# Performance work log

Measured on AMD Instinct MI355X. Metric: run time of the kernel, lower is better.

## Reference

```python
import jax, jax.numpy as jnp
import numpy as np

B, S, D = 4, 2048, 256


def setup_inputs() -> dict:
    key = jax.random.key(0)
    ks = jax.random.split(key, 8)
    context = jax.random.normal(ks[0], (B, S, D), dtype=jnp.float32)
    eos_mask = jax.random.randint(ks[1], (B, S, S), 0, 2, dtype=jnp.int32)
    prior = jax.random.uniform(ks[2], (B, S, S), dtype=jnp.float32)
    Wq = jax.random.normal(ks[3], (D, D), dtype=jnp.float32) * 0.02
    bq = jnp.zeros((D,), dtype=jnp.float32)
    Wk = jax.random.normal(ks[4], (D, D), dtype=jnp.float32) * 0.02
    bk = jnp.zeros((D,), dtype=jnp.float32)
    ln_a = jnp.ones((D,), dtype=jnp.float32)
    ln_b = jnp.zeros((D,), dtype=jnp.float32)
    return {"context": context, "prior": prior, "Wq": Wq, "bq": bq,
            "Wk": Wk, "bk": bk, "ln_a": ln_a, "ln_b": ln_b,
            "eos_mask": eos_mask}


def reference(context, prior, Wq, bq, Wk, bk, ln_a, ln_b, eos_mask):
    seq = context.shape[1]
    # LayerNorm (torch: unbiased std, eps added to std)
    mean = context.mean(axis=-1, keepdims=True)
    std = jnp.std(context, axis=-1, ddof=1, keepdims=True)
    x = ln_a * (context - mean) / (std + 1e-6) + ln_b

    idx = jnp.arange(seq)
    diff = idx[None, :] - idx[:, None]
    a = diff == 1                      # superdiagonal
    offdiag = jnp.abs(diff) == 1       # a + c (super + sub diagonal)
    eye = diff == 0                    # b
    tri = jnp.triu(jnp.ones((seq, seq), dtype=jnp.float32))

    # mask = eos_mask & (a + c)  (precedence: & binds looser than +)
    mask = jnp.bitwise_and(eos_mask, offdiag.astype(jnp.int32))

    # torch Linear: y = x @ W.T + b
    query = x @ Wq.T + bq
    key = x @ Wk.T + bk
    scores = jnp.einsum('bqd,bkd->bqk', query, key) / 256.0
    scores = jnp.where(mask == 0, -1e9, scores)
    neibor = jax.nn.softmax(scores, axis=-1)
    neibor = jnp.sqrt(neibor * neibor.transpose(0, 2, 1) + 1e-9)
    neibor = prior + (1.0 - prior) * neibor

    # log -> zero except superdiagonal -> triangular matmul -> exp
    t = jnp.where(a, jnp.log(neibor + 1e-9), 0.0) @ tri   # [B,S,S]
    g = jnp.exp(jnp.matmul(tri, t))                        # [B,S,S]
    strict_upper = jnp.logical_and(tri.astype(bool), jnp.logical_not(eye))
    g = jnp.where(strict_upper, g, 0.0)  # masked_fill(tri - b == 0, 0)
    g = g + g.transpose(0, 2, 1) + jnp.where(eye, neibor, 1e-9)
    return g
```

## Files before the change

kernel.cpp:

```cpp
#include <hip/hip_runtime.h>
#include <math.h>

#define SS 2048
#define DD 256
#define NB 4
#define NR (NB * SS)

__device__ __forceinline__ float block_sum(float v, float* sh) {
    int lane = threadIdx.x & 63;
    int wave = threadIdx.x >> 6;
#pragma unroll
    for (int off = 32; off > 0; off >>= 1) v += __shfl_down(v, off, 64);
    if (lane == 0) sh[wave] = v;
    __syncthreads();
    float r = sh[0] + sh[1] + sh[2] + sh[3];
    __syncthreads();
    return r;
}

__global__ __launch_bounds__(256) void prep_kernel(
    const float* __restrict__ Wq, const float* __restrict__ Wk,
    const float* __restrict__ bq, float* __restrict__ A, float* __restrict__ u) {
    int t = threadIdx.x;
    int d = blockIdx.x;
    if (d < DD) {
        float acc = 0.0f;
        for (int i = 0; i < DD; i++) acc += Wq[i * DD + d] * Wk[i * DD + t];
        A[d * DD + t] = acc;
    } else {
        float acc = 0.0f;
        for (int i = 0; i < DD; i++) acc += Wk[i * DD + t] * bq[i];
        u[t] = acc;
    }
}

__global__ __launch_bounds__(256) void ln_kernel(
    const float* __restrict__ ctx, const float* __restrict__ ln_a,
    const float* __restrict__ ln_b, float* __restrict__ xn) {
    __shared__ float sh[4];
    int r = blockIdx.x, t = threadIdx.x;
    float v = ctx[r * DD + t];
    float mean = block_sum(v, sh) * (1.0f / 256.0f);
    float d = v - mean;
    float s2 = block_sum(d * d, sh) * (1.0f / 255.0f);
    float inv = 1.0f / (sqrtf(s2) + 1e-6f);
    xn[r * DD + t] = ln_a[t] * d * inv + ln_b[t];
}

#define BM 64
#define BN 64
#define BK 16
__global__ __launch_bounds__(256) void gemm_kernel(
    const float* __restrict__ X, const float* __restrict__ A,
    const float* __restrict__ u, float* __restrict__ Y) {
    __shared__ float Xs[BK][BM + 1];
    __shared__ float As[BK][BN];
    int tid = threadIdx.x;
    int row0 = blockIdx.x * BM;
    int col0 = blockIdx.y * BN;
    int tx = tid & 15, ty = tid >> 4;
    float acc[4][4] = {};
    for (int k0 = 0; k0 < DD; k0 += BK) {
        {
            int m = tid >> 2;
            int kq = (tid & 3) * 4;
            float4 x4 = *(const float4*)(X + (size_t)(row0 + m) * DD + k0 + kq);
            Xs[kq + 0][m] = x4.x; Xs[kq + 1][m] = x4.y;
            Xs[kq + 2][m] = x4.z; Xs[kq + 3][m] = x4.w;
        }
        {
            int k = tid >> 4;
            int nq = (tid & 15) * 4;
            float4 a4 = *(const float4*)(A + (size_t)(k0 + k) * DD + col0 + nq);
            *(float4*)&As[k][nq] = a4;
        }
        __syncthreads();
#pragma unroll
        for (int k = 0; k < BK; k++) {
            float a[4], b[4];
#pragma unroll
            for (int i = 0; i < 4; i++) a[i] = Xs[k][ty * 4 + i];
#pragma unroll
            for (int j = 0; j < 4; j++) b[j] = As[k][tx * 4 + j];
#pragma unroll
            for (int i = 0; i < 4; i++)
#pragma unroll
                for (int j = 0; j < 4; j++) acc[i][j] += a[i] * b[j];
        }
        __syncthreads();
    }
    float4 uv = *(const float4*)(u + col0 + tx * 4);
#pragma unroll
    for (int i = 0; i < 4; i++) {
        float4 o = make_float4(acc[i][0] + uv.x, acc[i][1] + uv.y,
                               acc[i][2] + uv.z, acc[i][3] + uv.w);
        *(float4*)(Y + (size_t)(row0 + ty * 4 + i) * DD + col0 + tx * 4) = o;
    }
}

__global__ __launch_bounds__(256) void score_kernel(
    const float* __restrict__ Y, const float* __restrict__ xn,
    const int* __restrict__ eos, float4* __restrict__ pvals) {
    __shared__ float sh[4];
    int r = blockIdx.x, t = threadIdx.x;
    int s = r & (SS - 1), b = r >> 11;
    float yv = Y[(size_t)r * DD + t];
    bool has_n = (s < SS - 1), has_p = (s > 0);
    float xnext = has_n ? xn[(size_t)(r + 1) * DD + t] : 0.0f;
    float xprev = has_p ? xn[(size_t)(r - 1) * DD + t] : 0.0f;
    float dn = block_sum(yv * xnext, sh);
    float dp = block_sum(yv * xprev, sh);
    if (t == 0) {
        size_t base = (size_t)b * SS * SS + (size_t)s * SS;
        bool mn = has_n && ((eos[base + s + 1] & 1) != 0);
        bool mp = has_p && ((eos[base + s - 1] & 1) != 0);
        float pn, pp, pd;
        if (mn && mp) {
            float d = (dn - dp) * (1.0f / 256.0f);
            pn = 1.0f / (1.0f + expf(-d));
            pp = 1.0f / (1.0f + expf(d));
            pd = 0.0f;
        } else if (mn) { pn = 1.0f; pp = 0.0f; pd = 0.0f; }
        else if (mp)   { pn = 0.0f; pp = 1.0f; pd = 0.0f; }
        else           { pn = pp = pd = (1.0f / 2048.0f); }
        pvals[r] = make_float4(pn, pp, pd, 0.0f);
    }
}

__global__ __launch_bounds__(256) void scan_kernel(
    const float4* __restrict__ pvals, const float* __restrict__ prior,
    float* __restrict__ P) {
    int b = blockIdx.x, t = threadIdx.x;
    int base_s = t * 8;
    double loc[8];
    double run = 0.0;
#pragma unroll
    for (int i = 0; i < 8; i++) {
        loc[i] = run;
        int s = base_s + i;
        float lv = 0.0f;
        if (s < SS - 1) {
            int r = b * SS + s;
            float4 pv = pvals[r];
            float4 pv1 = pvals[r + 1];
            float ns = sqrtf(pv.x * pv1.y + 1e-9f);
            float pr = prior[(size_t)b * SS * SS + (size_t)s * SS + s + 1];
            float neib = pr + (1.0f - pr) * ns;
            lv = logf(neib + 1e-9f);
        }
        run += (double)lv;
    }
    int lane = t & 63, wave = t >> 6;
    double v = run;
#pragma unroll
    for (int off = 1; off < 64; off <<= 1) {
        double uu = __shfl_up(v, off, 64);
        if (lane >= off) v += uu;
    }
    __shared__ double wsum[4];
    if (lane == 63) wsum[wave] = v;
    __syncthreads();
    double woff = 0.0;
    for (int w = 0; w < wave; w++) woff += wsum[w];
    double texcl = woff + (v - run);
#pragma unroll
    for (int i = 0; i < 8; i++)
        P[b * SS + base_s + i] = (float)(texcl + loc[i]);
}

__global__ __launch_bounds__(256) void fill_kernel(
    const float* __restrict__ P, const float4* __restrict__ pvals,
    const float* __restrict__ prior, float* __restrict__ out) {
    int blk = blockIdx.x;
    int i = blk & (SS - 1), b = blk >> 11;
    int t = threadIdx.x;
    __shared__ float shPi, shDv;
    if (t == 0) {
        shPi = P[blk];
        float pd = pvals[blk].z;
        float prd = prior[(size_t)b * SS * SS + (size_t)i * SS + i];
        shDv = prd + (1.0f - prd) * sqrtf(pd * pd + 1e-9f);
    }
    __syncthreads();
    float Pi = shPi, dv = shDv;
    const float* Pb = P + b * SS;
    size_t outbase = (size_t)blk * SS;
    float4 pj0 = *(const float4*)(Pb + t * 8);
    float4 pj1 = *(const float4*)(Pb + t * 8 + 4);
    float pj[8] = {pj0.x, pj0.y, pj0.z, pj0.w, pj1.x, pj1.y, pj1.z, pj1.w};
    float res[8];
#pragma unroll
    for (int k = 0; k < 8; k++) {
        int j = t * 8 + k;
        float d = (j > i) ? (pj[k] - Pi) : (Pi - pj[k]);
        float val = expf(d) + 1e-9f;
        res[k] = (j == i) ? dv : val;
    }
    *(float4*)(out + outbase + t * 8) = make_float4(res[0], res[1], res[2], res[3]);
    *(float4*)(out + outbase + t * 8 + 4) = make_float4(res[4], res[5], res[6], res[7]);
}

extern "C" void kernel_launch(void* const* d_in, const int* in_sizes, int n_in,
                              void* d_out, int out_size, void* d_ws, size_t ws_size,
                              hipStream_t stream) {
    const float* context = (const float*)d_in[0];
    const float* prior   = (const float*)d_in[1];
    const float* Wq      = (const float*)d_in[2];
    const float* bq      = (const float*)d_in[3];
    const float* Wk      = (const float*)d_in[4];
    const float* ln_a    = (const float*)d_in[6];
    const float* ln_b    = (const float*)d_in[7];
    const int*   eos     = (const int*)d_in[8];
    float* out = (float*)d_out;

    float* ws = (float*)d_ws;
    float* xn    = ws;
    float* Y     = ws + 2097152;
    float* A     = ws + 4194304;
    float* u     = ws + 4259840;
    float4* pv   = (float4*)(ws + 4260096);
    float* P     = ws + 4292864;

    prep_kernel<<<DD + 1, 256, 0, stream>>>(Wq, Wk, bq, A, u);
    ln_kernel<<<NR, 256, 0, stream>>>(context, ln_a, ln_b, xn);
    gemm_kernel<<<dim3(NR / BM, DD / BN), 256, 0, stream>>>(xn, A, u, Y);
    score_kernel<<<NR, 256, 0, stream>>>(Y, xn, eos, pv);
    scan_kernel<<<NB, 256, 0, stream>>>(pv, prior, P);
    fill_kernel<<<NR, 256, 0, stream>>>(P, pv, prior, out);
}
```

Measured before the change: 226.8 us.

## Fuse projection GEMM with neighbor score dot products, wave-per-row layernorm

The projection GEMM and the neighbor score kernel are merged, so each block computes full 256-wide rows of Y and immediately dots them with (x_next - x_prev). This removes the Y intermediate buffer round trip and one launch. LayerNorm now uses one wave per row with float4 loads and shuffle reductions instead of block-wide shared-memory syncs, and expf is replaced by __expf in the fill and sigmoid paths. The eos mask test drops the &1 check and the fused GEMM gets less parallelism, with only 256 blocks.

```diff
diff --git a/kernel.cpp b/kernel.cpp
--- a/kernel.cpp
+++ b/kernel.cpp
@@ -5,18 +5,6 @@
 #define DD 256
 #define NB 4
 #define NR (NB * SS)
-
-__device__ __forceinline__ float block_sum(float v, float* sh) {
-    int lane = threadIdx.x & 63;
-    int wave = threadIdx.x >> 6;
-#pragma unroll
-    for (int off = 32; off > 0; off >>= 1) v += __shfl_down(v, off, 64);
-    if (lane == 0) sh[wave] = v;
-    __syncthreads();
-    float r = sh[0] + sh[1] + sh[2] + sh[3];
-    __syncthreads();
-    return r;
-}
 
 __global__ __launch_bounds__(256) void prep_kernel(
     const float* __restrict__ Wq, const float* __restrict__ Wk,
@@ -35,95 +23,115 @@
 }
 
 __global__ __launch_bounds__(256) void ln_kernel(
-    const float* __restrict__ ctx, const float* __restrict__ ln_a,
-    const float* __restrict__ ln_b, float* __restrict__ xn) {
-    __shared__ float sh[4];
-    int r = blockIdx.x, t = threadIdx.x;
-    float v = ctx[r * DD + t];
-    float mean = block_sum(v, sh) * (1.0f / 256.0f);
-    float d = v - mean;
-    float s2 = block_sum(d * d, sh) * (1.0f / 255.0f);
-    float inv = 1.0f / (sqrtf(s2) + 1e-6f);
-    xn[r * DD + t] = ln_a[t] * d * inv + ln_b[t];
-}
-
-#define BM 64
-#define BN 64
-#define BK 16
-__global__ __launch_bounds__(256) void gemm_kernel(
+    const float4* __restrict__ ctx4, const float4* __restrict__ ln_a4,
+    const float4* __restrict__ ln_b4, float4* __restrict__ xn4) {
+    int lane = threadIdx.x & 63;
+    int wave = threadIdx.x >> 6;
+    int r = blockIdx.x * 4 + wave;
+    float4 v = ctx4[(size_t)r * 64 + lane];
+    float s = v.x + v.y + v.z + v.w;
+#pragma unroll
+    for (int off = 32; off > 0; off >>= 1) s += __shfl_xor(s, off, 64);
+    float mean = s * (1.0f / 256.0f);
+    float4 d = make_float4(v.x - mean, v.y - mean, v.z - mean, v.w - mean);
+    float s2 = d.x * d.x + d.y * d.y + d.z * d.z + d.w * d.w;
+#pragma unroll
+    for (int off = 32; off > 0; off >>= 1) s2 += __shfl_xor(s2, off, 64);
+    float inv = 1.0f / (sqrtf(s2 * (1.0f / 255.0f)) + 1e-6f);
+    float4 ga = ln_a4[lane], gb = ln_b4[lane];
+    xn4[(size_t)r * 64 + lane] = make_float4(
+        ga.x * d.x * inv + gb.x, ga.y * d.y * inv + gb.y,
+        ga.z * d.z * inv + gb.z, ga.w * d.w * inv + gb.w);
+}
+
+#define BK 32
+#define FMA4(accv, a, bv) \
+    accv.x += (a) * bv.x; accv.y += (a) * bv.y; \
+    accv.z += (a) * bv.z; accv.w += (a) * bv.w;
+
+__global__ __launch_bounds__(256) void gemm_score_kernel(
     const float* __restrict__ X, const float* __restrict__ A,
-    const float* __restrict__ u, float* __restrict__ Y) {
-    __shared__ float Xs[BK][BM + 1];
-    __shared__ float As[BK][BN];
+    const float* __restrict__ u, const int* __restrict__ eos,
+    float4* __restrict__ pvals) {
+    __shared__ float Xs[BK][33];
+    __shared__ float As[BK][256];
     int tid = threadIdx.x;
-    int row0 = blockIdx.x * BM;
-    int col0 = blockIdx.y * BN;
     int tx = tid & 15, ty = tid >> 4;
-    float acc[4][4] = {};
+    int row0 = blockIdx.x * 32;
+    const float4* X4 = (const float4*)X;
+    const float4* A4 = (const float4*)A;
+
+    float4 acc[2][4] = {};
     for (int k0 = 0; k0 < DD; k0 += BK) {
         {
-            int m = tid >> 2;
-            int kq = (tid & 3) * 4;
-            float4 x4 = *(const float4*)(X + (size_t)(row0 + m) * DD + k0 + kq);
+            int m = tid >> 3;
+            int kq = (tid & 7) * 4;
+            float4 x4 = X4[(size_t)(row0 + m) * 64 + (k0 >> 2) + (tid & 7)];
             Xs[kq + 0][m] = x4.x; Xs[kq + 1][m] = x4.y;
             Xs[kq + 2][m] = x4.z; Xs[kq + 3][m] = x4.w;
         }
-        {
-            int k = tid >> 4;
-            int nq = (tid & 15) * 4;
-            float4 a4 = *(const float4*)(A + (size_t)(k0 + k) * DD + col0 + nq);
-            *(float4*)&As[k][nq] = a4;
+#pragma unroll
+        for (int q = 0; q < 8; q++) {
+            int f4 = q * 256 + tid;
+            int k = f4 >> 6, c4 = f4 & 63;
+            *(float4*)&As[k][c4 * 4] = A4[(size_t)(k0 + k) * 64 + c4];
         }
         __syncthreads();
 #pragma unroll
         for (int k = 0; k < BK; k++) {
-            float a[4], b[4];
-#pragma unroll
-            for (int i = 0; i < 4; i++) a[i] = Xs[k][ty * 4 + i];
-#pragma unroll
-            for (int j = 0; j < 4; j++) b[j] = As[k][tx * 4 + j];
-#pragma unroll
-            for (int i = 0; i < 4; i++)
-#pragma unroll
-                for (int j = 0; j < 4; j++) acc[i][j] += a[i] * b[j];
+            float a0 = Xs[k][ty * 2];
+            float a1 = Xs[k][ty * 2 + 1];
+            float4 b0 = *(const float4*)&As[k][tx * 4];
+            float4 b1 = *(const float4*)&As[k][tx * 4 + 64];
+            float4 b2 = *(const float4*)&As[k][tx * 4 + 128];
+            float4 b3 = *(const float4*)&As[k][tx * 4 + 192];
+            FMA4(acc[0][0], a0, b0) FMA4(acc[0][1], a0, b1)
+            FMA4(acc[0][2], a0, b2) FMA4(acc[0][3], a0, b3)
+            FMA4(acc[1][0], a1, b0) FMA4(acc[1][1], a1, b1)
+            FMA4(acc[1][2], a1, b2) FMA4(acc[1][3], a1, b3)
         }
         __syncthreads();
     }
-    float4 uv = *(const float4*)(u + col0 + tx * 4);
-#pragma unroll
-    for (int i = 0; i < 4; i++) {
-        float4 o = make_float4(acc[i][0] + uv.x, acc[i][1] + uv.y,
-                               acc[i][2] + uv.z, acc[i][3] + uv.w);
-        *(float4*)(Y + (size_t)(row0 + ty * 4 + i) * DD + col0 + tx * 4) = o;
-    }
-}
-
-__global__ __launch_bounds__(256) void score_kernel(
-    const float* __restrict__ Y, const float* __restrict__ xn,
-    const int* __restrict__ eos, float4* __restrict__ pvals) {
-    __shared__ float sh[4];
-    int r = blockIdx.x, t = threadIdx.x;
-    int s = r & (SS - 1), b = r >> 11;
-    float yv = Y[(size_t)r * DD + t];
-    bool has_n = (s < SS - 1), has_p = (s > 0);
-    float xnext = has_n ? xn[(size_t)(r + 1) * DD + t] : 0.0f;
-    float xprev = has_p ? xn[(size_t)(r - 1) * DD + t] : 0.0f;
-    float dn = block_sum(yv * xnext, sh);
-    float dp = block_sum(yv * xprev, sh);
-    if (t == 0) {
-        size_t base = (size_t)b * SS * SS + (size_t)s * SS;
-        bool mn = has_n && ((eos[base + s + 1] & 1) != 0);
-        bool mp = has_p && ((eos[base + s - 1] & 1) != 0);
-        float pn, pp, pd;
-        if (mn && mp) {
-            float d = (dn - dp) * (1.0f / 256.0f);
-            pn = 1.0f / (1.0f + expf(-d));
-            pp = 1.0f / (1.0f + expf(d));
-            pd = 0.0f;
-        } else if (mn) { pn = 1.0f; pp = 0.0f; pd = 0.0f; }
-        else if (mp)   { pn = 0.0f; pp = 1.0f; pd = 0.0f; }
-        else           { pn = pp = pd = (1.0f / 2048.0f); }
-        pvals[r] = make_float4(pn, pp, pd, 0.0f);
+    const float4* u4 = (const float4*)u;
+#pragma unroll
+    for (int q = 0; q < 4; q++) {
+        float4 uv = u4[q * 16 + tx];
+        acc[0][q].x += uv.x; acc[0][q].y += uv.y; acc[0][q].z += uv.z; acc[0][q].w += uv.w;
+        acc[1][q].x += uv.x; acc[1][q].y += uv.y; acc[1][q].z += uv.z; acc[1][q].w += uv.w;
+    }
+    const float4* xn4 = (const float4*)X;
+#pragma unroll
+    for (int i = 0; i < 2; i++) {
+        int r = row0 + ty * 2 + i;
+        int s = r & (SS - 1), b = r >> 11;
+        bool has_n = (s < SS - 1), has_p = (s > 0);
+        float partial = 0.0f;
+#pragma unroll
+        for (int q = 0; q < 4; q++) {
+            float4 wn = has_n ? xn4[(size_t)(r + 1) * 64 + q * 16 + tx]
+                              : make_float4(0, 0, 0, 0);
+            float4 wp = has_p ? xn4[(size_t)(r - 1) * 64 + q * 16 + tx]
+                              : make_float4(0, 0, 0, 0);
+            partial += acc[i][q].x * (wn.x - wp.x) + acc[i][q].y * (wn.y - wp.y)
+                     + acc[i][q].z * (wn.z - wp.z) + acc[i][q].w * (wn.w - wp.w);
+        }
+#pragma unroll
+        for (int off = 8; off > 0; off >>= 1) partial += __shfl_xor(partial, off, 64);
+        if (tx == 0) {
+            size_t base = (size_t)b * SS * SS + (size_t)s * SS;
+            bool mn = has_n && (eos[base + s + 1] != 0);
+            bool mp = has_p && (eos[base + s - 1] != 0);
+            float pn, pp, pd;
+            if (mn && mp) {
+                float d = partial * (1.0f / 256.0f);
+                pn = 1.0f / (1.0f + __expf(-d));
+                pp = 1.0f - pn;
+                pd = 0.0f;
+            } else if (mn) { pn = 1.0f; pp = 0.0f; pd = 0.0f; }
+            else if (mp)   { pn = 0.0f; pp = 1.0f; pd = 0.0f; }
+            else           { pn = pp = pd = (1.0f / 2048.0f); }
+            pvals[r] = make_float4(pn, pp, pd, 0.0f);
+        }
     }
 }
 
@@ -193,7 +201,7 @@
     for (int k = 0; k < 8; k++) {
         int j = t * 8 + k;
         float d = (j > i) ? (pj[k] - Pi) : (Pi - pj[k]);
-        float val = expf(d) + 1e-9f;
+        float val = __expf(d) + 1e-9f;
         res[k] = (j == i) ? dv : val;
     }
     *(float4*)(out + outbase + t * 8) = make_float4(res[0], res[1], res[2], res[3]);
@@ -215,16 +223,16 @@
 
     float* ws = (float*)d_ws;
     float* xn    = ws;
-    float* Y     = ws + 2097152;
     float* A     = ws + 4194304;
     float* u     = ws + 4259840;
     float4* pv   = (float4*)(ws + 4260096);
     float* P     = ws + 4292864;
 
     prep_kernel<<<DD + 1, 256, 0, stream>>>(Wq, Wk, bq, A, u);
-    ln_kernel<<<NR, 256, 0, stream>>>(context, ln_a, ln_b, xn);
-    gemm_kernel<<<dim3(NR / BM, DD / BN), 256, 0, stream>>>(xn, A, u, Y);
-    score_kernel<<<NR, 256, 0, stream>>>(Y, xn, eos, pv);
+    ln_kernel<<<NR / 4, 256, 0, stream>>>((const float4*)context,
+                                          (const float4*)ln_a,
+                                          (const float4*)ln_b, (float4*)xn);
+    gemm_score_kernel<<<NR / 32, 256, 0, stream>>>(xn, A, u, eos, pv);
     scan_kernel<<<NB, 256, 0, stream>>>(pv, prior, P);
     fill_kernel<<<NR, 256, 0, stream>>>(P, pv, prior, out);
 }
```

After: 220.5 us. 2.8% less time.
